# Kernel optimization log

Hardware: AMD Instinct MI355X
Metric: run time of the kernel (lower is better)

## Reference

```python
import jax, jax.numpy as jnp
import numpy as np

B, L, DIN, H, N, TEMB, NB = 16, 1024, 64, 256, 64, 128, 6


def setup_inputs() -> dict:
    key = jax.random.key(0)
    ks = jax.random.split(key, 16)
    def nrm(k, shape, scale):
        return jax.random.normal(k, shape, dtype=jnp.float32) * scale
    inp = {}
    inp["input"] = nrm(ks[0], (B, L, DIN), 1.0)
    inp["t"] = jax.random.uniform(ks[1], (B,), dtype=jnp.float32) * 1000.0
    inp["W_in"] = nrm(ks[2], (DIN, H), DIN ** -0.5)
    inp["b_in"] = jnp.zeros((H,), jnp.float32)
    inp["Wt1"] = nrm(ks[3], (TEMB, H), TEMB ** -0.5)
    inp["bt1"] = jnp.zeros((H,), jnp.float32)
    inp["Wt2"] = nrm(ks[4], (H, H), H ** -0.5)
    inp["bt2"] = jnp.zeros((H,), jnp.float32)
    inp["ln_g"] = jnp.ones((NB, H), jnp.float32)
    inp["ln_b"] = jnp.zeros((NB, H), jnp.float32)
    lo, hi = float(np.log(0.001)), float(np.log(0.1))
    inp["log_dt"] = jax.random.uniform(ks[5], (NB, H), dtype=jnp.float32) * (hi - lo) + lo
    inp["A_log_re"] = jnp.full((NB, H, N), float(np.log(0.5)), jnp.float32)
    inp["A_im"] = jnp.broadcast_to(np.pi * jnp.arange(N, dtype=jnp.float32), (NB, H, N)) + 0.0
    inp["C_re"] = nrm(ks[6], (NB, 2, H, N), 0.5 ** 0.5)
    inp["C_im"] = nrm(ks[7], (NB, 2, H, N), 0.5 ** 0.5)
    inp["Dp"] = nrm(ks[8], (NB, H), 1.0)
    inp["s4W"] = nrm(ks[9], (NB, H, H), H ** -0.5)
    inp["s4b"] = jnp.zeros((NB, H), jnp.float32)
    inp["tW"] = nrm(ks[10], (NB, H, H), H ** -0.5)
    inp["tb"] = jnp.zeros((NB, H), jnp.float32)
    inp["c1W"] = nrm(ks[11], (NB, H, H), H ** -0.5)
    inp["c1b"] = jnp.zeros((NB, H), jnp.float32)
    inp["c2W"] = nrm(ks[12], (NB, H, H), H ** -0.5)
    inp["c2b"] = jnp.zeros((NB, H), jnp.float32)
    inp["Wo1"] = nrm(ks[13], (H, H), H ** -0.5)
    inp["bo1"] = jnp.zeros((H,), jnp.float32)
    inp["Wo2"] = nrm(ks[14], (H, DIN), H ** -0.5)
    inp["bo2"] = jnp.zeros((DIN,), jnp.float32)
    return inp


def _sin_emb(t, dim):
    half = dim // 2
    freqs = jnp.exp(-np.log(10000.0) / (half - 1) * jnp.arange(half, dtype=jnp.float32))
    a = t[:, None] * freqs[None, :]
    return jnp.concatenate([jnp.sin(a), jnp.cos(a)], axis=-1)


def _forward(input, t, W_in, b_in, Wt1, bt1, Wt2, bt2, ln_g, ln_b, log_dt, A_log_re,
             A_im, C_re, C_im, Dp, s4W, s4b, tW, tb, c1W, c1b, c2W, c2b, Wo1, bo1, Wo2, bo2):
    x = jax.nn.relu(input @ W_in + b_in)                     # [B,L,H]
    tv = jax.nn.silu(_sin_emb(t, TEMB) @ Wt1 + bt1)
    tv = jax.nn.silu(tv @ Wt2 + bt2)                         # [B,H]
    x = jnp.swapaxes(x, -1, -2)                              # [B,H,L]
    length = x.shape[-1]
    nfft = 2 * length
    lgrid = jnp.arange(length)
    skips = jnp.zeros_like(x)
    for i in range(NB):
        # time conditioning (broadcast over L)
        tt = tv @ tW[i] + tb[i]                              # [B,H]
        z = x + tt[:, :, None]
        # LayerNorm over channel dim H
        zt = jnp.swapaxes(z, -1, -2)                         # [B,L,H]
        mu = zt.mean(-1, keepdims=True)
        var = zt.var(-1, keepdims=True)
        zn = (zt - mu) / jnp.sqrt(var + 1e-5) * ln_g[i] + ln_b[i]
        zn = jnp.swapaxes(zn, -1, -2)                        # [B,H,L]
        # S4 (diagonal ZOH) bidirectional convolution kernel
        dt = jnp.exp(log_dt[i])                              # [H]
        A = -jnp.exp(A_log_re[i]) + 1j * A_im[i]             # [H,N]
        dtA = A * dt[:, None]
        C = C_re[i] + 1j * C_im[i]                           # [2,H,N]
        dC = C * (jnp.exp(dtA) - 1.0) / A
        V = jnp.exp(dtA[:, :, None] * lgrid)                 # [H,N,L] Vandermonde
        K = 2.0 * jnp.einsum('shn,hnl->shl', dC, V).real     # [2,H,L]
        k = jnp.pad(K[0], ((0, 0), (0, length))) + jnp.pad(K[1][:, ::-1], ((0, 0), (length, 0)))
        y = jnp.fft.irfft(jnp.fft.rfft(zn, nfft) * jnp.fft.rfft(k, nfft)[None], nfft)[..., :length]
        y = y + zn * Dp[i][None, :, None]
        y = jax.nn.gelu(y, approximate=False)
        y = jnp.einsum('oh,bhl->bol', s4W[i], y) + s4b[i][None, :, None]
        out = y + z                                          # S4Layer residual
        g = jnp.tanh(out) * jax.nn.sigmoid(out)
        x = jnp.einsum('oh,bhl->bol', c1W[i], g) + c1b[i][None, :, None] + x
        skips = skips + jnp.einsum('oh,bhl->bol', c2W[i], g) + c2b[i][None, :, None]
    skip = jnp.swapaxes(skips, -1, -2)                       # [B,L,H]
    h = jax.nn.relu(skip @ Wo1 + bo1)
    out = h @ Wo2 + bo2
    return out + input                                       # init_skip


def reference(input, t, W_in, b_in, Wt1, bt1, Wt2, bt2, ln_g, ln_b, log_dt, A_log_re,
              A_im, C_re, C_im, Dp, s4W, s4b, tW, tb, c1W, c1b, c2W, c2b, Wo1, bo1, Wo2, bo2):
    return _forward(input, t, W_in, b_in, Wt1, bt1, Wt2, bt2, ln_g, ln_b, log_dt, A_log_re,
                    A_im, C_re, C_im, Dp, s4W, s4b, tW, tb, c1W, c1b, c2W, c2b, Wo1, bo1, Wo2, bo2)
```

## Files before the change

### kernel.cpp

```cpp
#include <hip/hip_runtime.h>
#include <math.h>


typedef __attribute__((ext_vector_type(8))) short bf16x8;
typedef __attribute__((ext_vector_type(4))) float f32x4;

__device__ __forceinline__ short f2bf(float f) {
  unsigned u = __builtin_bit_cast(unsigned, f);
  unsigned r = (u + 0x7FFFu + ((u >> 16) & 1u)) >> 16;
  return (short)r;
}
__device__ __forceinline__ float bf2f(unsigned short v) {
  unsigned u = ((unsigned)v) << 16;
  return __builtin_bit_cast(float, u);
}

__global__ __launch_bounds__(256) void k_temb(
    const float* __restrict__ t, const float* __restrict__ Wt1, const float* __restrict__ bt1,
    const float* __restrict__ Wt2, const float* __restrict__ bt2, float* __restrict__ tv) {
  int b = blockIdx.x, tid = threadIdx.x;
  __shared__ float emb[128];
  __shared__ float tv1[256];
  if (tid < 128) {
    int j = tid & 63;
// ... 14 lines not shown
__global__ __launch_bounds__(256) void k_tt(
    const float* __restrict__ tv, const float* __restrict__ tW, const float* __restrict__ tb,
    float* __restrict__ tt_all) {
  int i = blockIdx.x, b = blockIdx.y, h = threadIdx.x;
  __shared__ float s[256];
  s[h] = tv[b * 256 + h];
  __syncthreads();
  const float* W = tW + i * 256 * 256;
  float acc = tb[i * 256 + h];
  for (int k = 0; k < 256; k++) acc = fmaf(s[k], W[k * 256 + h], acc);
  tt_all[(i * 16 + b) * 256 + h] = acc;
}

__global__ __launch_bounds__(256) void k_in(
    const float* __restrict__ inp, const float* __restrict__ W, const float* __restrict__ bias,
    float* __restrict__ x) {
  int lt = blockIdx.x, b = blockIdx.y, h = threadIdx.x;
  __shared__ float si[64][68];
  int l0 = lt * 64;
  for (int rep = 0; rep < 16; rep++) {
    int idx = rep * 256 + h;
    int l = idx >> 6, d = idx & 63;
    si[l][d] = inp[(size_t)(b * 1024 + l0 + l) * 64 + d];
  }
  float wc[64];
  #pragma unroll
  for (int d = 0; d < 64; d++) wc[d] = W[d * 256 + h];
  float bh = bias[h];
  __syncthreads();
  float* xp = x + (size_t)(b * 256 + h) * 1024 + l0;
  for (int l4 = 0; l4 < 16; l4++) {
    float4 o;
    float* op = &o.x;
    #pragma unroll
    for (int j = 0; j < 4; j++) {
      int l = l4 * 4 + j;
      float a = bh;
      #pragma unroll
      for (int d4 = 0; d4 < 16; d4++) {
        float4 v = *reinterpret_cast<const float4*>(&si[l][d4 * 4]);
        a = fmaf(v.x, wc[d4 * 4 + 0], a);
        a = fmaf(v.y, wc[d4 * 4 + 1], a);
        a = fmaf(v.z, wc[d4 * 4 + 2], a);
        a = fmaf(v.w, wc[d4 * 4 + 3], a);
      }
      op[j] = fmaxf(a, 0.f);
    }
    *reinterpret_cast<float4*>(xp + l4 * 4) = o;
  }
}

__global__ __launch_bounds__(256) void k_tab(
    const float* __restrict__ log_dt, const float* __restrict__ A_log_re, const float* __restrict__ A_im,
    const float* __restrict__ C_re, const float* __restrict__ C_im,
    float* __restrict__ wtab, float* __restrict__ wTtab, float* __restrict__ dCtab) {
  int idx = blockIdx.x * 256 + threadIdx.x;
  int i = idx / (256 * 64);
  int rem = idx % (256 * 64);
  int h = rem >> 6, n = rem & 63;
  float dt = expf(log_dt[i * 256 + h]);
  float Ar = -expf(A_log_re[idx]);
  float Ai = A_im[idx];
  float ar = dt * Ar, ai = dt * Ai;
// ... 25 lines not shown
    s4Wbf[idx] = (unsigned short)f2bf(s4W[idx]);
  } else if (idx < 393216 + 786432) {
    int j = idx - 393216;
    int i = j / 131072, r = j % 131072;
    int o2 = r >> 8, k = r & 255;
    float v = (o2 < 256) ? c1W[(size_t)i * 65536 + o2 * 256 + k]
                         : c2W[(size_t)i * 65536 + (o2 - 256) * 256 + k];
    c12Wbf[j] = (unsigned short)f2bf(v);
  } else {
    int j = idx - 1179648;
    int o = j >> 8, k = j & 255;
    Wo1T[j] = (unsigned short)f2bf(Wo1[k * 256 + o]);
  }
}

__global__ __launch_bounds__(256) void k_conv(const float* __restrict__ src, unsigned short* __restrict__ dst) {
  int idx = (blockIdx.x * 256 + threadIdx.x) * 8;
  float4 v0 = *reinterpret_cast<const float4*>(src + idx);
  float4 v1 = *reinterpret_cast<const float4*>(src + idx + 4);
  ushort4 a = make_ushort4((unsigned short)f2bf(v0.x), (unsigned short)f2bf(v0.y),
                           (unsigned short)f2bf(v0.z), (unsigned short)f2bf(v0.w));
  ushort4 b = make_ushort4((unsigned short)f2bf(v1.x), (unsigned short)f2bf(v1.y),
                           (unsigned short)f2bf(v1.z), (unsigned short)f2bf(v1.w));
  *reinterpret_cast<ushort4*>(dst + idx) = a;
  *reinterpret_cast<ushort4*>(dst + idx + 4) = b;
}

__global__ __launch_bounds__(256) void k_pcar(const float* __restrict__ wtab, float* __restrict__ Pt) {
  int idx = blockIdx.x * 256 + threadIdx.x;
  int i = idx >> 14, h = (idx >> 6) & 255, n = idx & 63;
  float wr = wtab[idx * 2], wi = wtab[idx * 2 + 1];
  float pr = 1.f, pi = 0.f;
  float* base = Pt + (size_t)i * 2097152 + (size_t)h * 8192 + 2 * n;
  for (int t = 0; t < 64; t++) {
    *reinterpret_cast<float2*>(base + t * 128) = make_float2(pr, -pi);
    float nr2 = pr * wr - pi * wi, ni2 = pr * wi + pi * wr;
    pr = nr2; pi = ni2;
  }
}

__global__ __launch_bounds__(256) void k_ktap(
    const float* __restrict__ dCtab, const float* __restrict__ Pt, float* __restrict__ Ktap) {
  int idx = blockIdx.x * 256 + threadIdx.x;
  int j = idx & 63;
  int h = (idx >> 6) & 255;
  int i = idx >> 15;
  const float* dc = dCtab + (size_t)(idx >> 6) * 128;
  const float* P = Pt + (size_t)i * 2097152 + (size_t)h * 8192 + j * 128;
  float acc = 0.f;
  for (int q = 0; q < 32; q++) {
    float4 d = *reinterpret_cast<const float4*>(dc + q * 4);
    float4 p = *reinterpret_cast<const float4*>(P + q * 4);
    acc = fmaf(d.x, p.x, fmaf(d.y, p.y, fmaf(d.z, p.z, fmaf(d.w, p.w, acc))));
  }
  Ktap[idx] = 2.f * acc;
}

__global__ __launch_bounds__(256) void k_ln(
    const float* __restrict__ x, const float* __restrict__ tt_all,
    const float* __restrict__ g, const float* __restrict__ bta, unsigned short* __restrict__ znbf, int i) {
  int ct = blockIdx.x, b = blockIdx.y, tid = threadIdx.x;
  __shared__ float tile[64][257];
  __shared__ float stt[256];
  __shared__ float red[8][64];
  __shared__ float mu_s[64], rs_s[64];
  stt[tid] = tt_all[(i * 16 + b) * 256 + tid];
  __syncthreads();
  int l0 = ct * 64;
  const float* xb = x + (size_t)(b * 256) * 1024 + l0;
  for (int rep = 0; rep < 16; rep++) {
    int idx = rep * 256 + tid;
    int h = idx >> 4;
    int l4 = (idx & 15) * 4;
    float4 v = *reinterpret_cast<const float4*>(xb + (size_t)h * 1024 + l4);
    float a = stt[h];
    tile[l4][h] = v.x + a; tile[l4 + 1][h] = v.y + a; tile[l4 + 2][h] = v.z + a; tile[l4 + 3][h] = v.w + a;
  }
  __syncthreads();
  int l = tid & 63, part = tid >> 6;
  float s1 = 0.f, s2 = 0.f;
  for (int k = 0; k < 64; k++) {
    float v = tile[l][part * 64 + k];
    s1 += v; s2 = fmaf(v, v, s2);
  }
  red[part][l] = s1; red[4 + part][l] = s2;
  __syncthreads();
  if (tid < 64) {
    float a = red[0][tid] + red[1][tid] + red[2][tid] + red[3][tid];
    float q = red[4][tid] + red[5][tid] + red[6][tid] + red[7][tid];
    float mu = a * (1.f / 256.f);
    float var = q * (1.f / 256.f) - mu * mu;
    mu_s[tid] = mu;
    rs_s[tid] = rsqrtf(var + 1e-5f);
  }
  __syncthreads();
  unsigned short* zb = znbf + (size_t)(b * 256) * 1024 + l0;
  for (int rep = 0; rep < 16; rep++) {
    int idx = rep * 256 + tid;
    int h = idx >> 4;
    int l4 = (idx & 15) * 4;
    float gg = g[i * 256 + h], bb2 = bta[i * 256 + h];
    float o0 = (tile[l4][h]     - mu_s[l4])     * rs_s[l4]     * gg + bb2;
    float o1 = (tile[l4 + 1][h] - mu_s[l4 + 1]) * rs_s[l4 + 1] * gg + bb2;
    float o2 = (tile[l4 + 2][h] - mu_s[l4 + 2]) * rs_s[l4 + 2] * gg + bb2;
    float o3 = (tile[l4 + 3][h] - mu_s[l4 + 3]) * rs_s[l4 + 3] * gg + bb2;
    ushort4 o4 = make_ushort4((unsigned short)f2bf(o0), (unsigned short)f2bf(o1),
                              (unsigned short)f2bf(o2), (unsigned short)f2bf(o3));
    *reinterpret_cast<ushort4*>(zb + (size_t)h * 1024 + l4) = o4;
  }
}

__global__ __launch_bounds__(512, 1) void k_s4(
    const unsigned short* __restrict__ znbf, const float* __restrict__ Pt,
    const float* __restrict__ wtab, const float* __restrict__ wTtab, const float* __restrict__ dCtab,
    const float* __restrict__ Ktap, const float* __restrict__ Dp,
    unsigned short* __restrict__ ygbf, int i) {
  int h = blockIdx.x;
  int tid = threadIdx.x;
  __shared__ unsigned short Psb[64][130];
  __shared__ unsigned short XR[22016];
  __shared__ unsigned short Sw[8][2][16][136];
  __shared__ float k0s[64], k1s[64];

  if (tid < 64) k0s[tid] = Ktap[h * 64 + tid];
  else if (tid < 128) k1s[tid - 64] = Ktap[16384 + h * 64 + (tid - 64)];

  {
    const float* src = Pt + (size_t)h * 8192;
    #pragma unroll
    for (int rep = 0; rep < 4; rep++) {
      int idx = rep * 512 + tid;
      int t = idx >> 5, k4 = (idx & 31) * 4;
      float4 v = *reinterpret_cast<const float4*>(src + t * 128 + k4);
      ushort2 a = make_ushort2((unsigned short)f2bf(v.x), (unsigned short)f2bf(v.y));
      ushort2 bq = make_ushort2((unsigned short)f2bf(v.z), (unsigned short)f2bf(v.w));
      *reinterpret_cast<ushort2*>(&Psb[t][k4]) = a;
      *reinterpret_cast<ushort2*>(&Psb[t][k4 + 2]) = bq;
    }
  }
  __syncthreads();
  {
    int t = tid & 63;
    int colblk = tid >> 6;
    #pragma unroll
    for (int cc = 0; cc < 32; cc++) {
      int col = colblk * 32 + cc;
      int n = col & 63, comp = (col >> 6) & 1, dir = col >> 7;
      int k = 2 * n + comp;
      unsigned short v = dir ? Psb[t][k] : Psb[63 - t][k];
      if (comp) v ^= 0x8000u;
      XR[col * 72 + t] = v;
    }
  }
  __syncthreads();

  int wid = tid >> 6, lane = tid & 63;
  int b = blockIdx.y * 8 + wid;
  int c = lane & 15, kq = lane >> 4;
  const unsigned short* pzn = znbf + ((size_t)(b * 256 + h)) * 1024 + c * 64 + kq * 8;

  bf16x8 af0 = *reinterpret_cast<const bf16x8*>(pzn);
  bf16x8 af1 = *reinterpret_cast<const bf16x8*>(pzn + 32);

  f32x4 acc[16];
  #pragma unroll
  for (int nt = 0; nt < 16; nt++) acc[nt] = (f32x4){0.f, 0.f, 0.f, 0.f};
  #pragma unroll
  for (int nt = 0; nt < 16; nt++) {
    bf16x8 b0 = *reinterpret_cast<const bf16x8*>(&XR[(nt * 16 + c) * 72 + kq * 8]);
    acc[nt] = __builtin_amdgcn_mfma_f32_16x16x32_bf16(af0, b0, acc[nt], 0, 0, 0);
  }
  #pragma unroll
  for (int nt = 0; nt < 16; nt++) {
    bf16x8 b1 = *reinterpret_cast<const bf16x8*>(&XR[(nt * 16 + c) * 72 + 32 + kq * 8]);
    acc[nt] = __builtin_amdgcn_mfma_f32_16x16x32_bf16(af1, b1, acc[nt], 0, 0, 0);
  }
  __syncthreads();

  {
    int trow = tid >> 6, klane = tid & 63;
    #pragma unroll
    for (int ti = 0; ti < 8; ti++) {
      int t = ti * 8 + trow;
      #pragma unroll
      for (int kc = 0; kc < 5; kc++) {
        int k = kc * 64 + klane;
        unsigned short v;
        if (kc < 2)      v = Psb[t][k];
        else if (kc < 4) v = Psb[63 - t][k - 128];
        else {
          int tp = klane;
          float f = (t >= tp) ? k0s[t - tp] : k1s[tp - t - 1];
          v = (unsigned short)f2bf(f);
        }
        XR[t * 344 + k] = v;
      }
    }
  }

  unsigned short* swf = &Sw[wid][0][0][0];
  unsigned short* swb = &Sw[wid][1][0][0];
  const int gib = (i * 256 + h) * 64;
  #pragma unroll
  for (int j = 0; j < 4; j++) {
    int n = j * 16 + c;
    int gi = gib + n;
    float wTr = wTtab[gi * 2], wTi = wTtab[gi * 2 + 1];
    float w2r = wTr * wTr - wTi * wTi, w2i = 2.f * wTr * wTi;
    float w4r = w2r * w2r - w2i * w2i, w4i = 2.f * w2r * w2i;
    float w8r = w4r * w4r - w4i * w4i, w8i = 2.f * w4r * w4i;
    float wr = wtab[gi * 2], wi = wtab[gi * 2 + 1];
    float d0r = dCtab[((size_t)(i * 2 + 0) * 256 + h) * 128 + 2 * n];
    float d0i = dCtab[((size_t)(i * 2 + 0) * 256 + h) * 128 + 2 * n + 1];
    float d1r = dCtab[((size_t)(i * 2 + 1) * 256 + h) * 128 + 2 * n];
    float d1i = dCtab[((size_t)(i * 2 + 1) * 256 + h) * 128 + 2 * n + 1];
    float mfr = 2.f * (d0r * wr - d0i * wi), mfi = 2.f * (d0r * wi + d0i * wr);
    float mbr = 2.f * d1r, mbi = 2.f * d1i;

    {
      float er = 0.f, ei = 0.f, entr[4], enti[4];
      #pragma unroll
      for (int r = 0; r < 4; r++) {
        entr[r] = er; enti[r] = ei;
        float br = acc[j][r], bi = acc[j + 4][r];
        float t0 = er * wTr - ei * wTi + br;
        ei = er * wTi + ei * wTr + bi; er = t0;
      }
      float Gr = er, Gi = ei;
      float sr = __shfl_up(Gr, 16), si = __shfl_up(Gi, 16);
      if (kq >= 1) { Gr += sr * w4r - si * w4i; Gi += sr * w4i + si * w4r; }
      sr = __shfl_up(Gr, 32); si = __shfl_up(Gi, 32);
      if (kq >= 2) { Gr += sr * w8r - si * w8i; Gi += sr * w8i + si * w8r; }
      float Sgr = __shfl_up(Gr, 16), Sgi = __shfl_up(Gi, 16);
      if (kq == 0) { Sgr = 0.f; Sgi = 0.f; }
      float pr = 1.f, pi = 0.f;
      #pragma unroll
      for (int r = 0; r < 4; r++) {
        float scr = pr * Sgr - pi * Sgi + entr[r];
        float sci = pr * Sgi + pi * Sgr + enti[r];
        float opr = mfr * scr - mfi * sci;
        float opi = mfr * sci + mfi * scr;
        *reinterpret_cast<ushort2*>(swf + (kq * 4 + r) * 136 + 2 * n) =
            make_ushort2((unsigned short)f2bf(opr), (unsigned short)f2bf(opi));
        float t0 = pr * wTr - pi * wTi; pi = pr * wTi + pi * wTr; pr = t0;
      }
    }
    {
      float er = 0.f, ei = 0.f, entr[4], enti[4];
      #pragma unroll
      for (int rr = 0; rr < 4; rr++) {
        int r = 3 - rr;
        entr[r] = er; enti[r] = ei;
        float br = acc[8 + j][r], bi = acc[12 + j][r];
        float t0 = er * wTr - ei * wTi + br;
        ei = er * wTi + ei * wTr + bi; er = t0;
      }
      float Gr = er, Gi = ei;
      float sr = __shfl_down(Gr, 16), si = __shfl_down(Gi, 16);
      if (kq <= 2) { Gr += sr * w4r - si * w4i; Gi += sr * w4i + si * w4r; }
      sr = __shfl_down(Gr, 32); si = __shfl_down(Gi, 32);
      if (kq <= 1) { Gr += sr * w8r - si * w8i; Gi += sr * w8i + si * w8r; }
      float Sgr = __shfl_down(Gr, 16), Sgi = __shfl_down(Gi, 16);
      if (kq == 3) { Sgr = 0.f; Sgi = 0.f; }
      float pr = 1.f, pi = 0.f;
      #pragma unroll
      for (int rr = 0; rr < 4; rr++) {
        int r = 3 - rr;
        float scr = pr * Sgr - pi * Sgi + entr[r];
        float sci = pr * Sgi + pi * Sgr + enti[r];
        float opr = mbr * scr - mbi * sci;
        float opi = mbr * sci + mbi * scr;
        *reinterpret_cast<ushort2*>(swb + (kq * 4 + r) * 136 + 2 * n) =
            make_ushort2((unsigned short)f2bf(opr), (unsigned short)f2bf(opi));
        float t0 = pr * wTr - pi * wTi; pi = pr * wTi + pi * wTr; pr = t0;
      }
    }
  }
  __syncthreads();

  f32x4 acc2[4];
  #pragma unroll
  for (int nt = 0; nt < 4; nt++) acc2[nt] = (f32x4){0.f, 0.f, 0.f, 0.f};
  #pragma unroll
  for (int ks = 0; ks < 10; ks++) {
    bf16x8 af;
    if (ks < 4)       af = *reinterpret_cast<const bf16x8*>(swf + c * 136 + ks * 32 + kq * 8);
    else if (ks < 8)  af = *reinterpret_cast<const bf16x8*>(swb + c * 136 + (ks - 4) * 32 + kq * 8);
    else              af = *reinterpret_cast<const bf16x8*>(pzn + (ks - 8) * 32);
    #pragma unroll
    for (int nt = 0; nt < 4; nt++) {
      bf16x8 bfv = *reinterpret_cast<const bf16x8*>(&XR[(nt * 16 + c) * 344 + ks * 32 + kq * 8]);
      acc2[nt] = __builtin_amdgcn_mfma_f32_16x16x32_bf16(af, bfv, acc2[nt], 0, 0, 0);
    }
  }

  float dp = Dp[i * 256 + h];
  size_t obase = (size_t)(b * 256 + h) * 1024;
  #pragma unroll
  for (int nt = 0; nt < 4; nt++) {
    #pragma unroll
    for (int r = 0; r < 4; r++) {
      int m = kq * 4 + r;
      int t = nt * 16 + c;
      size_t idx = obase + (size_t)m * 64 + t;
      float z = bf2f(znbf[idx]);
      float v = fmaf(z, dp, acc2[nt][r]);
      float gel = 0.5f * v * (1.f + erff(v * 0.70710678118f));
      ygbf[idx] = (unsigned short)f2bf(gel);
    }
  }
}

template <int EPI>
__global__ __launch_bounds__(256) void k_gemm(
    const unsigned short* __restrict__ Wbf, const float* __restrict__ bias1, const float* __restrict__ bias2,
    const unsigned short* __restrict__ act, float* __restrict__ out1, float* __restrict__ out2,
    unsigned short* __restrict__ outb, const float* __restrict__ aux1, const float* __restrict__ aux2) {
  int lt = blockIdx.x, ot = blockIdx.y, b = blockIdx.z;
  int tid = threadIdx.x;
  int l0 = lt * 128, o0 = ot * 64;
  __shared__ unsigned short Alds[128 * 40];

  int wid = tid >> 6, lane = tid & 63;
  int wo = wid >> 1, wl = wid & 1;
  int c = lane & 15, kq = lane >> 4;

  int kq4 = tid >> 5;
  int lq = tid & 31;
  const unsigned short* actb = act + (size_t)(b * 256) * 1024 + l0 + lq * 4;

  f32x4 acc[2][4];
  #pragma unroll
// ... 50 lines not shown
        acc[mo][nl] = __builtin_amdgcn_mfma_f32_16x16x32_bf16(af[mo], bfr[nl], acc[mo][nl], 0, 0, 0);
    __syncthreads();
  }

  #pragma unroll
  for (int mo = 0; mo < 2; mo++) {
    #pragma unroll
    for (int nl = 0; nl < 4; nl++) {
      #pragma unroll
      for (int r = 0; r < 4; r++) {
        float a = acc[mo][nl][r];
        int o = o0 + wo * 32 + mo * 16 + kq * 4 + r;
        int l = l0 + wl * 64 + nl * 16 + c;
        if constexpr (EPI == 0) {
          size_t id = ((size_t)(b * 256 + o)) * 1024 + l;
          float u = a + bias1[o] + aux1[id] + aux2[b * 256 + o];
          float t = __expf(fminf(-u, 80.f));
          float gg = (1.f - t) / (1.f + t * t);
          outb[id] = (unsigned short)f2bf(gg);
        } else if constexpr (EPI == 1 || EPI == 4) {
          if (o < 256) {
            size_t id = ((size_t)(b * 256 + o)) * 1024 + l;
            out1[id] += a + bias1[o];
          } else {
            int o2 = o - 256;
            size_t id = ((size_t)(b * 256 + o2)) * 1024 + l;
            if constexpr (EPI == 4) out2[id] = a + bias2[o2];
            else                    out2[id] += a + bias2[o2];
          }
        } else {
          size_t id = ((size_t)(b * 256 + o)) * 1024 + l;
          out1[id] = fmaxf(a + bias1[o], 0.f);
        }
      }
    }
  }
}

__global__ __launch_bounds__(256) void k_out(
    const float* __restrict__ h1, const float* __restrict__ Wo2, const float* __restrict__ bo2,
    const float* __restrict__ inp, float* __restrict__ outp) {
  int lt = blockIdx.x, b = blockIdx.y, tid = threadIdx.x;
  __shared__ float sa[32][132];
  __shared__ float sw2[32][68];
  int l0 = lt * 128;
  float acc[4][8];
  #pragma unroll
  for (int r = 0; r < 4; r++)
    #pragma unroll
    for (int c2 = 0; c2 < 8; c2++) acc[r][c2] = 0.f;
  int df = (tid & 7) * 8;
  int lf = (tid >> 3) * 4;
  for (int kc = 0; kc < 256; kc += 32) {
    for (int rep = 0; rep < 4; rep++) {
      int idx = rep * 256 + tid;
      int kk = idx >> 5;
      int l4 = (idx & 31) * 4;
      float4 v = *reinterpret_cast<const float4*>(h1 + (size_t)(b * 256 + kc + kk) * 1024 + l0 + l4);
      *reinterpret_cast<float4*>(&sa[kk][l4]) = v;
    }
    for (int rep = 0; rep < 8; rep++) {
      int idx = rep * 256 + tid;
      int kk = idx >> 6, d = idx & 63;
      sw2[kk][d] = Wo2[(size_t)(kc + kk) * 64 + d];
    }
    __syncthreads();
    for (int kk = 0; kk < 32; kk++) {
      float4 av = *reinterpret_cast<const float4*>(&sa[kk][lf]);
      float4 w1 = *reinterpret_cast<const float4*>(&sw2[kk][df]);
      float4 w2 = *reinterpret_cast<const float4*>(&sw2[kk][df + 4]);
      float avv[4] = {av.x, av.y, av.z, av.w};
      float wv[8] = {w1.x, w1.y, w1.z, w1.w, w2.x, w2.y, w2.z, w2.w};
      #pragma unroll
      for (int r = 0; r < 4; r++)
// ... 41 lines not shown
  const float* s4W     = (const float*)d_in[16];
  const float* s4b     = (const float*)d_in[17];
  const float* tW      = (const float*)d_in[18];
  const float* tb      = (const float*)d_in[19];
  const float* c1W     = (const float*)d_in[20];
  const float* c1b     = (const float*)d_in[21];
  const float* c2W     = (const float*)d_in[22];
  const float* c2b     = (const float*)d_in[23];
  const float* Wo1     = (const float*)d_in[24];
  const float* bo1     = (const float*)d_in[25];
  const float* Wo2     = (const float*)d_in[26];
  const float* bo2     = (const float*)d_in[27];

  float* ws = (float*)d_ws;
  size_t off = 0;
  float* x      = ws + off; off += 4194304;
  float* zn     = ws + off; off += 4194304;
  float* ygbuf  = ws + off; off += 4194304;
  float* skips  = ws + off; off += 4194304;
  float* tv     = ws + off; off += 4096;
  float* tt_all = ws + off; off += 24576;
  float* wtab   = ws + off; off += 196608;
  float* wTtab  = ws + off; off += 196608;
  float* dCtab  = ws + off; off += 393216;
  float* Pt     = ws + off; off += 12582912;
  float* Ktap   = ws + off; off += 196608;
  unsigned short* s4Wbf  = (unsigned short*)(ws + off); off += 196608;
  unsigned short* c12Wbf = (unsigned short*)(ws + off); off += 393216;
  unsigned short* Wo1T   = (unsigned short*)(ws + off); off += 32768;

  unsigned short* znbf    = (unsigned short*)zn;
  unsigned short* ygbf    = (unsigned short*)ygbuf;
  unsigned short* gbf     = (unsigned short*)(ygbuf + 2097152);
  unsigned short* skipsbf = (unsigned short*)x;
  float* h1 = zn;

  k_temb<<<16, 256, 0, stream>>>(t, Wt1, bt1, Wt2, bt2, tv);
  k_tt<<<dim3(6, 16), 256, 0, stream>>>(tv, tW, tb, tt_all);
  k_in<<<dim3(16, 16), 256, 0, stream>>>(input, W_in, b_in, x);
  k_tab<<<384, 256, 0, stream>>>(log_dt, A_log_re, A_im, C_re, C_im, wtab, wTtab, dCtab);
  k_prep<<<4864, 256, 0, stream>>>(s4W, c1W, c2W, Wo1, s4Wbf, c12Wbf, Wo1T);
  k_pcar<<<384, 256, 0, stream>>>(wtab, Pt);
  k_ktap<<<768, 256, 0, stream>>>(dCtab, Pt, Ktap);

  for (int i = 0; i < 6; i++) {
    k_ln<<<dim3(16, 16), 256, 0, stream>>>(x, tt_all, ln_g, ln_b, znbf, i);
    k_s4<<<dim3(256, 2), 512, 0, stream>>>(znbf, Pt + (size_t)i * 2097152, wtab, wTtab, dCtab,
                                           Ktap + (size_t)i * 32768, Dp, ygbf, i);
    k_gemm<0><<<dim3(8, 4, 16), 256, 0, stream>>>(s4Wbf + (size_t)i * 65536, s4b + i * 256, nullptr,
                                                  ygbf, nullptr, nullptr, gbf, x, tt_all + i * 4096);
    if (i == 0)
      k_gemm<4><<<dim3(8, 8, 16), 256, 0, stream>>>(c12Wbf, c1b, c2b, gbf, x, skips,
                                                    nullptr, nullptr, nullptr);
    else
      k_gemm<1><<<dim3(8, 8, 16), 256, 0, stream>>>(c12Wbf + (size_t)i * 131072, c1b + i * 256,
                                                    c2b + i * 256, gbf, x, skips,
                                                    nullptr, nullptr, nullptr);
  }
  k_conv<<<2048, 256, 0, stream>>>(skips, skipsbf);
  k_gemm<2><<<dim3(8, 4, 16), 256, 0, stream>>>(Wo1T, bo1, nullptr,
                                                skipsbf, h1, nullptr, nullptr, nullptr, nullptr);
  k_out<<<dim3(8, 16), 256, 0, stream>>>(h1, Wo2, bo2, input, (float*)d_out);
}
```

Measured before the change: 580.2 us.

## Store residual, skip, and S4 power tables in bf16 and restructure S4 blocks

The residual stream x, the skip accumulator, h1, and the Pt power table are now stored as bf16 instead of fp32. This roughly halves global memory traffic in the LN, GEMM epilogue, S4, and output kernels and removes the separate skip-conversion kernel. The S4 kernel now launches one block per channel that handles both batch halves, so the Pt/Toeplitz shared-memory setup is built once and reused. The cost is accuracy: the residual and skip sums are re-rounded to bf16 after every layer's accumulation, which may drift beyond tolerance.

Measured after the change: 790.0 us. 1.36x slower.

```diff
diff --git a/kernel.cpp b/kernel.cpp
--- a/kernel.cpp
+++ b/kernel.cpp
@@ -52,7 +52,7 @@
 
 __global__ __launch_bounds__(256) void k_in(
     const float* __restrict__ inp, const float* __restrict__ W, const float* __restrict__ bias,
-    float* __restrict__ x) {
+    unsigned short* __restrict__ xbf) {
   int lt = blockIdx.x, b = blockIdx.y, h = threadIdx.x;
   __shared__ float si[64][68];
   int l0 = lt * 64;
@@ -66,10 +66,9 @@
   for (int d = 0; d < 64; d++) wc[d] = W[d * 256 + h];
   float bh = bias[h];
   __syncthreads();
-  float* xp = x + (size_t)(b * 256 + h) * 1024 + l0;
+  unsigned short* xp = xbf + (size_t)(b * 256 + h) * 1024 + l0;
   for (int l4 = 0; l4 < 16; l4++) {
-    float4 o;
-    float* op = &o.x;
+    float op[4];
     #pragma unroll
     for (int j = 0; j < 4; j++) {
       int l = l4 * 4 + j;
@@ -84,7 +83,9 @@
       }
       op[j] = fmaxf(a, 0.f);
     }
-    *reinterpret_cast<float4*>(xp + l4 * 4) = o;
+    ushort4 o = make_ushort4((unsigned short)f2bf(op[0]), (unsigned short)f2bf(op[1]),
+                             (unsigned short)f2bf(op[2]), (unsigned short)f2bf(op[3]));
+    *reinterpret_cast<ushort4*>(xp + l4 * 4) = o;
   }
 }
 
@@ -140,73 +141,65 @@
   }
 }
 
-__global__ __launch_bounds__(256) void k_conv(const float* __restrict__ src, unsigned short* __restrict__ dst) {
-  int idx = (blockIdx.x * 256 + threadIdx.x) * 8;
-  float4 v0 = *reinterpret_cast<const float4*>(src + idx);
-  float4 v1 = *reinterpret_cast<const float4*>(src + idx + 4);
-  ushort4 a = make_ushort4((unsigned short)f2bf(v0.x), (unsigned short)f2bf(v0.y),
-                           (unsigned short)f2bf(v0.z), (unsigned short)f2bf(v0.w));
-  ushort4 b = make_ushort4((unsigned short)f2bf(v1.x), (unsigned short)f2bf(v1.y),
-                           (unsigned short)f2bf(v1.z), (unsigned short)f2bf(v1.w));
-  *reinterpret_cast<ushort4*>(dst + idx) = a;
-  *reinterpret_cast<ushort4*>(dst + idx + 4) = b;
-}
-
-__global__ __launch_bounds__(256) void k_pcar(const float* __restrict__ wtab, float* __restrict__ Pt) {
+__global__ __launch_bounds__(256) void k_pcar(const float* __restrict__ wtab, unsigned short* __restrict__ Ptb) {
   int idx = blockIdx.x * 256 + threadIdx.x;
   int i = idx >> 14, h = (idx >> 6) & 255, n = idx & 63;
   float wr = wtab[idx * 2], wi = wtab[idx * 2 + 1];
   float pr = 1.f, pi = 0.f;
-  float* base = Pt + (size_t)i * 2097152 + (size_t)h * 8192 + 2 * n;
+  unsigned short* base = Ptb + (size_t)i * 2097152 + (size_t)h * 8192 + 2 * n;
   for (int t = 0; t < 64; t++) {
-    *reinterpret_cast<float2*>(base + t * 128) = make_float2(pr, -pi);
+    *reinterpret_cast<ushort2*>(base + t * 128) =
+        make_ushort2((unsigned short)f2bf(pr), (unsigned short)f2bf(-pi));
     float nr2 = pr * wr - pi * wi, ni2 = pr * wi + pi * wr;
     pr = nr2; pi = ni2;
   }
 }
 
 __global__ __launch_bounds__(256) void k_ktap(
-    const float* __restrict__ dCtab, const float* __restrict__ Pt, float* __restrict__ Ktap) {
+    const float* __restrict__ dCtab, const unsigned short* __restrict__ Ptb, float* __restrict__ Ktap) {
   int idx = blockIdx.x * 256 + threadIdx.x;
   int j = idx & 63;
   int h = (idx >> 6) & 255;
   int i = idx >> 15;
   const float* dc = dCtab + (size_t)(idx >> 6) * 128;
-  const float* P = Pt + (size_t)i * 2097152 + (size_t)h * 8192 + j * 128;
+  const unsigned short* P = Ptb + (size_t)i * 2097152 + (size_t)h * 8192 + j * 128;
   float acc = 0.f;
   for (int q = 0; q < 32; q++) {
     float4 d = *reinterpret_cast<const float4*>(dc + q * 4);
-    float4 p = *reinterpret_cast<const float4*>(P + q * 4);
-    acc = fmaf(d.x, p.x, fmaf(d.y, p.y, fmaf(d.z, p.z, fmaf(d.w, p.w, acc))));
+    ushort4 p = *reinterpret_cast<const ushort4*>(P + q * 4);
+    acc = fmaf(d.x, bf2f(p.x), fmaf(d.y, bf2f(p.y), fmaf(d.z, bf2f(p.z), fmaf(d.w, bf2f(p.w), acc))));
   }
   Ktap[idx] = 2.f * acc;
 }
 
 __global__ __launch_bounds__(256) void k_ln(
-    const float* __restrict__ x, const float* __restrict__ tt_all,
+    const unsigned short* __restrict__ xbf, const float* __restrict__ tt_all,
     const float* __restrict__ g, const float* __restrict__ bta, unsigned short* __restrict__ znbf, int i) {
   int ct = blockIdx.x, b = blockIdx.y, tid = threadIdx.x;
-  __shared__ float tile[64][257];
+  __shared__ unsigned short tile[64][266];
   __shared__ float stt[256];
   __shared__ float red[8][64];
   __shared__ float mu_s[64], rs_s[64];
   stt[tid] = tt_all[(i * 16 + b) * 256 + tid];
   __syncthreads();
   int l0 = ct * 64;
-  const float* xb = x + (size_t)(b * 256) * 1024 + l0;
+  const unsigned short* xb = xbf + (size_t)(b * 256) * 1024 + l0;
   for (int rep = 0; rep < 16; rep++) {
     int idx = rep * 256 + tid;
     int h = idx >> 4;
     int l4 = (idx & 15) * 4;
-    float4 v = *reinterpret_cast<const float4*>(xb + (size_t)h * 1024 + l4);
+    ushort4 v = *reinterpret_cast<const ushort4*>(xb + (size_t)h * 1024 + l4);
     float a = stt[h];
-    tile[l4][h] = v.x + a; tile[l4 + 1][h] = v.y + a; tile[l4 + 2][h] = v.z + a; tile[l4 + 3][h] = v.w + a;
+    tile[l4][h]     = (unsigned short)f2bf(bf2f(v.x) + a);
+    tile[l4 + 1][h] = (unsigned short)f2bf(bf2f(v.y) + a);
+    tile[l4 + 2][h] = (unsigned short)f2bf(bf2f(v.z) + a);
+    tile[l4 + 3][h] = (unsigned short)f2bf(bf2f(v.w) + a);
   }
   __syncthreads();
   int l = tid & 63, part = tid >> 6;
   float s1 = 0.f, s2 = 0.f;
   for (int k = 0; k < 64; k++) {
-    float v = tile[l][part * 64 + k];
+    float v = bf2f(tile[l][part * 64 + k]);
     s1 += v; s2 = fmaf(v, v, s2);
   }
   red[part][l] = s1; red[4 + part][l] = s2;
@@ -226,10 +219,10 @@
     int h = idx >> 4;
     int l4 = (idx & 15) * 4;
     float gg = g[i * 256 + h], bb2 = bta[i * 256 + h];
-    float o0 = (tile[l4][h]     - mu_s[l4])     * rs_s[l4]     * gg + bb2;
-    float o1 = (tile[l4 + 1][h] - mu_s[l4 + 1]) * rs_s[l4 + 1] * gg + bb2;
-    float o2 = (tile[l4 + 2][h] - mu_s[l4 + 2]) * rs_s[l4 + 2] * gg + bb2;
-    float o3 = (tile[l4 + 3][h] - mu_s[l4 + 3]) * rs_s[l4 + 3] * gg + bb2;
+    float o0 = (bf2f(tile[l4][h])     - mu_s[l4])     * rs_s[l4]     * gg + bb2;
+    float o1 = (bf2f(tile[l4 + 1][h]) - mu_s[l4 + 1]) * rs_s[l4 + 1] * gg + bb2;
+    float o2 = (bf2f(tile[l4 + 2][h]) - mu_s[l4 + 2]) * rs_s[l4 + 2] * gg + bb2;
+    float o3 = (bf2f(tile[l4 + 3][h]) - mu_s[l4 + 3]) * rs_s[l4 + 3] * gg + bb2;
     ushort4 o4 = make_ushort4((unsigned short)f2bf(o0), (unsigned short)f2bf(o1),
                               (unsigned short)f2bf(o2), (unsigned short)f2bf(o3));
     *reinterpret_cast<ushort4*>(zb + (size_t)h * 1024 + l4) = o4;
@@ -237,31 +230,28 @@
 }
 
 __global__ __launch_bounds__(512, 1) void k_s4(
-    const unsigned short* __restrict__ znbf, const float* __restrict__ Pt,
+    const unsigned short* __restrict__ znbf, const unsigned short* __restrict__ Ptb,
     const float* __restrict__ wtab, const float* __restrict__ wTtab, const float* __restrict__ dCtab,
     const float* __restrict__ Ktap, const float* __restrict__ Dp,
     unsigned short* __restrict__ ygbf, int i) {
   int h = blockIdx.x;
   int tid = threadIdx.x;
-  __shared__ unsigned short Psb[64][130];
-  __shared__ unsigned short XR[22016];
-  __shared__ unsigned short Sw[8][2][16][136];
+  __shared__ unsigned short Bp[256 * 72];
+  __shared__ unsigned short Blds[64 * 344];
+  __shared__ unsigned short SwA[34816];
   __shared__ float k0s[64], k1s[64];
 
   if (tid < 64) k0s[tid] = Ktap[h * 64 + tid];
   else if (tid < 128) k1s[tid - 64] = Ktap[16384 + h * 64 + (tid - 64)];
 
   {
-    const float* src = Pt + (size_t)h * 8192;
+    const unsigned short* src = Ptb + (size_t)h * 8192;
     #pragma unroll
     for (int rep = 0; rep < 4; rep++) {
-      int idx = rep * 512 + tid;
-      int t = idx >> 5, k4 = (idx & 31) * 4;
-      float4 v = *reinterpret_cast<const float4*>(src + t * 128 + k4);
-      ushort2 a = make_ushort2((unsigned short)f2bf(v.x), (unsigned short)f2bf(v.y));
-      ushort2 bq = make_ushort2((unsigned short)f2bf(v.z), (unsigned short)f2bf(v.w));
-      *reinterpret_cast<ushort2*>(&Psb[t][k4]) = a;
-      *reinterpret_cast<ushort2*>(&Psb[t][k4 + 2]) = bq;
+      int idx4 = (rep * 512 + tid) * 4;
+      int t = idx4 >> 7, k = idx4 & 127;
+      ushort4 v = *reinterpret_cast<const ushort4*>(src + idx4);
+      *reinterpret_cast<ushort4*>(&SwA[t * 132 + k]) = v;
     }
   }
   __syncthreads();
@@ -273,60 +263,38 @@
       int col = colblk * 32 + cc;
       int n = col & 63, comp = (col >> 6) & 1, dir = col >> 7;
       int k = 2 * n + comp;
-      unsigned short v = dir ? Psb[t][k] : Psb[63 - t][k];
+      unsigned short v = dir ? SwA[t * 132 + k] : SwA[(63 - t) * 132 + k];
       if (comp) v ^= 0x8000u;
-      XR[col * 72 + t] = v;
-    }
-  }
-  __syncthreads();
-
-  int wid = tid >> 6, lane = tid & 63;
-  int b = blockIdx.y * 8 + wid;
-  int c = lane & 15, kq = lane >> 4;
-  const unsigned short* pzn = znbf + ((size_t)(b * 256 + h)) * 1024 + c * 64 + kq * 8;
-
-  bf16x8 af0 = *reinterpret_cast<const bf16x8*>(pzn);
-  bf16x8 af1 = *reinterpret_cast<const bf16x8*>(pzn + 32);
-
-  f32x4 acc[16];
-  #pragma unroll
-  for (int nt = 0; nt < 16; nt++) acc[nt] = (f32x4){0.f, 0.f, 0.f, 0.f};
-  #pragma unroll
-  for (int nt = 0; nt < 16; nt++) {
-    bf16x8 b0 = *reinterpret_cast<const bf16x8*>(&XR[(nt * 16 + c) * 72 + kq * 8]);
-    acc[nt] = __builtin_amdgcn_mfma_f32_16x16x32_bf16(af0, b0, acc[nt], 0, 0, 0);
-  }
-  #pragma unroll
-  for (int nt = 0; nt < 16; nt++) {
-    bf16x8 b1 = *reinterpret_cast<const bf16x8*>(&XR[(nt * 16 + c) * 72 + 32 + kq * 8]);
-    acc[nt] = __builtin_amdgcn_mfma_f32_16x16x32_bf16(af1, b1, acc[nt], 0, 0, 0);
-  }
-  __syncthreads();
-
-  {
+      Bp[col * 72 + t] = v;
+    }
     int trow = tid >> 6, klane = tid & 63;
     #pragma unroll
     for (int ti = 0; ti < 8; ti++) {
-      int t = ti * 8 + trow;
+      int t2 = ti * 8 + trow;
       #pragma unroll
       for (int kc = 0; kc < 5; kc++) {
         int k = kc * 64 + klane;
         unsigned short v;
-        if (kc < 2)      v = Psb[t][k];
-        else if (kc < 4) v = Psb[63 - t][k - 128];
+        if (kc < 2)      v = SwA[t2 * 132 + k];
+        else if (kc < 4) v = SwA[(63 - t2) * 132 + (k - 128)];
         else {
           int tp = klane;
-          float f = (t >= tp) ? k0s[t - tp] : k1s[tp - t - 1];
+          float f = (t2 >= tp) ? k0s[t2 - tp] : k1s[tp - t2 - 1];
           v = (unsigned short)f2bf(f);
         }
-        XR[t * 344 + k] = v;
+        Blds[t2 * 344 + k] = v;
       }
     }
   }
-
-  unsigned short* swf = &Sw[wid][0][0][0];
-  unsigned short* swb = &Sw[wid][1][0][0];
+  __syncthreads();
+
+  int wid = tid >> 6, lane = tid & 63;
+  int c = lane & 15, kq = lane >> 4;
+  unsigned short* swf = &SwA[(wid * 2 + 0) * 2176];
+  unsigned short* swb = &SwA[(wid * 2 + 1) * 2176];
   const int gib = (i * 256 + h) * 64;
+
+  float wTr_[4], wTi_[4], w4r_[4], w4i_[4], w8r_[4], w8i_[4], mfr_[4], mfi_[4], mbr_[4], mbi_[4];
   #pragma unroll
   for (int j = 0; j < 4; j++) {
     int n = j * 16 + c;
@@ -334,105 +302,134 @@
     float wTr = wTtab[gi * 2], wTi = wTtab[gi * 2 + 1];
     float w2r = wTr * wTr - wTi * wTi, w2i = 2.f * wTr * wTi;
     float w4r = w2r * w2r - w2i * w2i, w4i = 2.f * w2r * w2i;
-    float w8r = w4r * w4r - w4i * w4i, w8i = 2.f * w4r * w4i;
+    w8r_[j] = w4r * w4r - w4i * w4i; w8i_[j] = 2.f * w4r * w4i;
+    w4r_[j] = w4r; w4i_[j] = w4i;
+    wTr_[j] = wTr; wTi_[j] = wTi;
     float wr = wtab[gi * 2], wi = wtab[gi * 2 + 1];
     float d0r = dCtab[((size_t)(i * 2 + 0) * 256 + h) * 128 + 2 * n];
     float d0i = dCtab[((size_t)(i * 2 + 0) * 256 + h) * 128 + 2 * n + 1];
     float d1r = dCtab[((size_t)(i * 2 + 1) * 256 + h) * 128 + 2 * n];
     float d1i = dCtab[((size_t)(i * 2 + 1) * 256 + h) * 128 + 2 * n + 1];
-    float mfr = 2.f * (d0r * wr - d0i * wi), mfi = 2.f * (d0r * wi + d0i * wr);
-    float mbr = 2.f * d1r, mbi = 2.f * d1i;
-
-    {
-      float er = 0.f, ei = 0.f, entr[4], enti[4];
+    mfr_[j] = 2.f * (d0r * wr - d0i * wi); mfi_[j] = 2.f * (d0r * wi + d0i * wr);
+    mbr_[j] = 2.f * d1r; mbi_[j] = 2.f * d1i;
+  }
+  float dp = Dp[i * 256 + h];
+
+  for (int bq = 0; bq < 2; bq++) {
+    int b = bq * 8 + wid;
+    const unsigned short* pzn = znbf + ((size_t)(b * 256 + h)) * 1024 + c * 64 + kq * 8;
+    bf16x8 af0 = *reinterpret_cast<const bf16x8*>(pzn);
+    bf16x8 af1 = *reinterpret_cast<const bf16x8*>(pzn + 32);
+
+    f32x4 acc[16];
+    #pragma unroll
+    for (int nt = 0; nt < 16; nt++) acc[nt] = (f32x4){0.f, 0.f, 0.f, 0.f};
+    #pragma unroll
+    for (int nt = 0; nt < 16; nt++) {
+      bf16x8 b0 = *reinterpret_cast<const bf16x8*>(&Bp[(nt * 16 + c) * 72 + kq * 8]);
+      acc[nt] = __builtin_amdgcn_mfma_f32_16x16x32_bf16(af0, b0, acc[nt], 0, 0, 0);
+    }
+    #pragma unroll
+    for (int nt = 0; nt < 16; nt++) {
+      bf16x8 b1 = *reinterpret_cast<const bf16x8*>(&Bp[(nt * 16 + c) * 72 + 32 + kq * 8]);
+      acc[nt] = __builtin_amdgcn_mfma_f32_16x16x32_bf16(af1, b1, acc[nt], 0, 0, 0);
+    }
+
+    #pragma unroll
+    for (int j = 0; j < 4; j++) {
+      int n = j * 16 + c;
+      float wTr = wTr_[j], wTi = wTi_[j];
+      float w4r = w4r_[j], w4i = w4i_[j], w8r = w8r_[j], w8i = w8i_[j];
+      float mfr = mfr_[j], mfi = mfi_[j], mbr = mbr_[j], mbi = mbi_[j];
+      {
+        float er = 0.f, ei = 0.f, entr[4], enti[4];
+        #pragma unroll
+        for (int r = 0; r < 4; r++) {
+          entr[r] = er; enti[r] = ei;
+          float br = acc[j][r], bi = acc[j + 4][r];
+          float t0 = er * wTr - ei * wTi + br;
+          ei = er * wTi + ei * wTr + bi; er = t0;
+        }
+        float Gr = er, Gi = ei;
+        float sr = __shfl_up(Gr, 16), si = __shfl_up(Gi, 16);
+        if (kq >= 1) { Gr += sr * w4r - si * w4i; Gi += sr * w4i + si * w4r; }
+        sr = __shfl_up(Gr, 32); si = __shfl_up(Gi, 32);
+        if (kq >= 2) { Gr += sr * w8r - si * w8i; Gi += sr * w8i + si * w8r; }
+        float Sgr = __shfl_up(Gr, 16), Sgi = __shfl_up(Gi, 16);
+        if (kq == 0) { Sgr = 0.f; Sgi = 0.f; }
+        float pr = 1.f, pi = 0.f;
+        #pragma unroll
+        for (int r = 0; r < 4; r++) {
+          float scr = pr * Sgr - pi * Sgi + entr[r];
+          float sci = pr * Sgi + pi * Sgr + enti[r];
+          float opr = mfr * scr - mfi * sci;
+          float opi = mfr * sci + mfi * scr;
+          *reinterpret_cast<ushort2*>(swf + (kq * 4 + r) * 136 + 2 * n) =
+              make_ushort2((unsigned short)f2bf(opr), (unsigned short)f2bf(opi));
+          float t0 = pr * wTr - pi * wTi; pi = pr * wTi + pi * wTr; pr = t0;
+        }
+      }
+      {
+        float er = 0.f, ei = 0.f, entr[4], enti[4];
+        #pragma unroll
+        for (int rr = 0; rr < 4; rr++) {
+          int r = 3 - rr;
+          entr[r] = er; enti[r] = ei;
+          float br = acc[8 + j][r], bi = acc[12 + j][r];
+          float t0 = er * wTr - ei * wTi + br;
+          ei = er * wTi + ei * wTr + bi; er = t0;
+        }
+        float Gr = er, Gi = ei;
+        float sr = __shfl_down(Gr, 16), si = __shfl_down(Gi, 16);
+        if (kq <= 2) { Gr += sr * w4r - si * w4i; Gi += sr * w4i + si * w4r; }
+        sr = __shfl_down(Gr, 32); si = __shfl_down(Gi, 32);
+        if (kq <= 1) { Gr += sr * w8r - si * w8i; Gi += sr * w8i + si * w8r; }
+        float Sgr = __shfl_down(Gr, 16), Sgi = __shfl_down(Gi, 16);
+        if (kq == 3) { Sgr = 0.f; Sgi = 0.f; }
+        float pr = 1.f, pi = 0.f;
+        #pragma unroll
+        for (int rr = 0; rr < 4; rr++) {
+          int r = 3 - rr;
+          float scr = pr * Sgr - pi * Sgi + entr[r];
+          float sci = pr * Sgi + pi * Sgr + enti[r];
+          float opr = mbr * scr - mbi * sci;
+          float opi = mbr * sci + mbi * scr;
+          *reinterpret_cast<ushort2*>(swb + (kq * 4 + r) * 136 + 2 * n) =
+              make_ushort2((unsigned short)f2bf(opr), (unsigned short)f2bf(opi));
+          float t0 = pr * wTr - pi * wTi; pi = pr * wTi + pi * wTr; pr = t0;
+        }
+      }
+    }
+
+    f32x4 acc2[4];
+    #pragma unroll
+    for (int nt = 0; nt < 4; nt++) acc2[nt] = (f32x4){0.f, 0.f, 0.f, 0.f};
+    #pragma unroll
+    for (int ks = 0; ks < 10; ks++) {
+      bf16x8 af;
+      if (ks < 4)       af = *reinterpret_cast<const bf16x8*>(swf + c * 136 + ks * 32 + kq * 8);
+      else if (ks < 8)  af = *reinterpret_cast<const bf16x8*>(swb + c * 136 + (ks - 4) * 32 + kq * 8);
+      else              af = *reinterpret_cast<const bf16x8*>(pzn + (ks - 8) * 32);
+      #pragma unroll
+      for (int nt = 0; nt < 4; nt++) {
+        bf16x8 bfv = *reinterpret_cast<const bf16x8*>(&Blds[(nt * 16 + c) * 344 + ks * 32 + kq * 8]);
+        acc2[nt] = __builtin_amdgcn_mfma_f32_16x16x32_bf16(af, bfv, acc2[nt], 0, 0, 0);
+      }
+    }
+
+    size_t obase = (size_t)(b * 256 + h) * 1024;
+    #pragma unroll
+    for (int nt = 0; nt < 4; nt++) {
       #pragma unroll
       for (int r = 0; r < 4; r++) {
-        entr[r] = er; enti[r] = ei;
-        float br = acc[j][r], bi = acc[j + 4][r];
-        float t0 = er * wTr - ei * wTi + br;
-        ei = er * wTi + ei * wTr + bi; er = t0;
+        int m = kq * 4 + r;
+        int t = nt * 16 + c;
+        size_t idx = obase + (size_t)m * 64 + t;
+        float z = bf2f(znbf[idx]);
+        float v = fmaf(z, dp, acc2[nt][r]);
+        float gel = 0.5f * v * (1.f + erff(v * 0.70710678118f));
+        ygbf[idx] = (unsigned short)f2bf(gel);
       }
-      float Gr = er, Gi = ei;
-      float sr = __shfl_up(Gr, 16), si = __shfl_up(Gi, 16);
-      if (kq >= 1) { Gr += sr * w4r - si * w4i; Gi += sr * w4i + si * w4r; }
-      sr = __shfl_up(Gr, 32); si = __shfl_up(Gi, 32);
-      if (kq >= 2) { Gr += sr * w8r - si * w8i; Gi += sr * w8i + si * w8r; }
-      float Sgr = __shfl_up(Gr, 16), Sgi = __shfl_up(Gi, 16);
-      if (kq == 0) { Sgr = 0.f; Sgi = 0.f; }
-      float pr = 1.f, pi = 0.f;
-      #pragma unroll
-      for (int r = 0; r < 4; r++) {
-        float scr = pr * Sgr - pi * Sgi + entr[r];
-        float sci = pr * Sgi + pi * Sgr + enti[r];
-        float opr = mfr * scr - mfi * sci;
-        float opi = mfr * sci + mfi * scr;
-        *reinterpret_cast<ushort2*>(swf + (kq * 4 + r) * 136 + 2 * n) =
-            make_ushort2((unsigned short)f2bf(opr), (unsigned short)f2bf(opi));
-        float t0 = pr * wTr - pi * wTi; pi = pr * wTi + pi * wTr; pr = t0;
-      }
-    }
-    {
-      float er = 0.f, ei = 0.f, entr[4], enti[4];
-      #pragma unroll
-      for (int rr = 0; rr < 4; rr++) {
-        int r = 3 - rr;
-        entr[r] = er; enti[r] = ei;
-        float br = acc[8 + j][r], bi = acc[12 + j][r];
-        float t0 = er * wTr - ei * wTi + br;
-        ei = er * wTi + ei * wTr + bi; er = t0;
-      }
-      float Gr = er, Gi = ei;
-      float sr = __shfl_down(Gr, 16), si = __shfl_down(Gi, 16);
-      if (kq <= 2) { Gr += sr * w4r - si * w4i; Gi += sr * w4i + si * w4r; }
-      sr = __shfl_down(Gr, 32); si = __shfl_down(Gi, 32);
-      if (kq <= 1) { Gr += sr * w8r - si * w8i; Gi += sr * w8i + si * w8r; }
-      float Sgr = __shfl_down(Gr, 16), Sgi = __shfl_down(Gi, 16);
-      if (kq == 3) { Sgr = 0.f; Sgi = 0.f; }
-      float pr = 1.f, pi = 0.f;
-      #pragma unroll
-      for (int rr = 0; rr < 4; rr++) {
-        int r = 3 - rr;
-        float scr = pr * Sgr - pi * Sgi + entr[r];
-        float sci = pr * Sgi + pi * Sgr + enti[r];
-        float opr = mbr * scr - mbi * sci;
-        float opi = mbr * sci + mbi * scr;
-        *reinterpret_cast<ushort2*>(swb + (kq * 4 + r) * 136 + 2 * n) =
-            make_ushort2((unsigned short)f2bf(opr), (unsigned short)f2bf(opi));
-        float t0 = pr * wTr - pi * wTi; pi = pr * wTi + pi * wTr; pr = t0;
-      }
-    }
-  }
-  __syncthreads();
-
-  f32x4 acc2[4];
-  #pragma unroll
-  for (int nt = 0; nt < 4; nt++) acc2[nt] = (f32x4){0.f, 0.f, 0.f, 0.f};
-  #pragma unroll
-  for (int ks = 0; ks < 10; ks++) {
-    bf16x8 af;
-    if (ks < 4)       af = *reinterpret_cast<const bf16x8*>(swf + c * 136 + ks * 32 + kq * 8);
-    else if (ks < 8)  af = *reinterpret_cast<const bf16x8*>(swb + c * 136 + (ks - 4) * 32 + kq * 8);
-    else              af = *reinterpret_cast<const bf16x8*>(pzn + (ks - 8) * 32);
-    #pragma unroll
-    for (int nt = 0; nt < 4; nt++) {
-      bf16x8 bfv = *reinterpret_cast<const bf16x8*>(&XR[(nt * 16 + c) * 344 + ks * 32 + kq * 8]);
-      acc2[nt] = __builtin_amdgcn_mfma_f32_16x16x32_bf16(af, bfv, acc2[nt], 0, 0, 0);
-    }
-  }
-
-  float dp = Dp[i * 256 + h];
-  size_t obase = (size_t)(b * 256 + h) * 1024;
-  #pragma unroll
-  for (int nt = 0; nt < 4; nt++) {
-    #pragma unroll
-    for (int r = 0; r < 4; r++) {
-      int m = kq * 4 + r;
-      int t = nt * 16 + c;
-      size_t idx = obase + (size_t)m * 64 + t;
-      float z = bf2f(znbf[idx]);
-      float v = fmaf(z, dp, acc2[nt][r]);
-      float gel = 0.5f * v * (1.f + erff(v * 0.70710678118f));
-      ygbf[idx] = (unsigned short)f2bf(gel);
     }
   }
 }
@@ -440,8 +437,8 @@
 template <int EPI>
 __global__ __launch_bounds__(256) void k_gemm(
     const unsigned short* __restrict__ Wbf, const float* __restrict__ bias1, const float* __restrict__ bias2,
-    const unsigned short* __restrict__ act, float* __restrict__ out1, float* __restrict__ out2,
-    unsigned short* __restrict__ outb, const float* __restrict__ aux1, const float* __restrict__ aux2) {
+    const unsigned short* __restrict__ act, unsigned short* __restrict__ uio1, unsigned short* __restrict__ uio2,
+    unsigned short* __restrict__ outb, const unsigned short* __restrict__ aux1, const float* __restrict__ aux2) {
   int lt = blockIdx.x, ot = blockIdx.y, b = blockIdx.z;
   int tid = threadIdx.x;
   int l0 = lt * 128, o0 = ot * 64;
@@ -522,23 +519,23 @@
         int l = l0 + wl * 64 + nl * 16 + c;
         if constexpr (EPI == 0) {
           size_t id = ((size_t)(b * 256 + o)) * 1024 + l;
-          float u = a + bias1[o] + aux1[id] + aux2[b * 256 + o];
+          float u = a + bias1[o] + bf2f(aux1[id]) + aux2[b * 256 + o];
           float t = __expf(fminf(-u, 80.f));
           float gg = (1.f - t) / (1.f + t * t);
           outb[id] = (unsigned short)f2bf(gg);
         } else if constexpr (EPI == 1 || EPI == 4) {
           if (o < 256) {
             size_t id = ((size_t)(b * 256 + o)) * 1024 + l;
-            out1[id] += a + bias1[o];
+            uio1[id] = (unsigned short)f2bf(bf2f(uio1[id]) + a + bias1[o]);
           } else {
             int o2 = o - 256;
             size_t id = ((size_t)(b * 256 + o2)) * 1024 + l;
-            if constexpr (EPI == 4) out2[id] = a + bias2[o2];
-            else                    out2[id] += a + bias2[o2];
+            if constexpr (EPI == 4) uio2[id] = (unsigned short)f2bf(a + bias2[o2]);
+            else                    uio2[id] = (unsigned short)f2bf(bf2f(uio2[id]) + a + bias2[o2]);
           }
         } else {
           size_t id = ((size_t)(b * 256 + o)) * 1024 + l;
-          out1[id] = fmaxf(a + bias1[o], 0.f);
+          outb[id] = (unsigned short)f2bf(fmaxf(a + bias1[o], 0.f));
         }
       }
     }
@@ -546,7 +543,7 @@
 }
 
 __global__ __launch_bounds__(256) void k_out(
-    const float* __restrict__ h1, const float* __restrict__ Wo2, const float* __restrict__ bo2,
+    const unsigned short* __restrict__ h1, const float* __restrict__ Wo2, const float* __restrict__ bo2,
     const float* __restrict__ inp, float* __restrict__ outp) {
   int lt = blockIdx.x, b = blockIdx.y, tid = threadIdx.x;
   __shared__ float sa[32][132];
@@ -564,8 +561,9 @@
       int idx = rep * 256 + tid;
       int kk = idx >> 5;
       int l4 = (idx & 31) * 4;
-      float4 v = *reinterpret_cast<const float4*>(h1 + (size_t)(b * 256 + kc + kk) * 1024 + l0 + l4);
-      *reinterpret_cast<float4*>(&sa[kk][l4]) = v;
+      ushort4 v = *reinterpret_cast<const ushort4*>(h1 + (size_t)(b * 256 + kc + kk) * 1024 + l0 + l4);
+      sa[kk][l4] = bf2f(v.x); sa[kk][l4 + 1] = bf2f(v.y);
+      sa[kk][l4 + 2] = bf2f(v.z); sa[kk][l4 + 3] = bf2f(v.w);
     }
     for (int rep = 0; rep < 8; rep++) {
       int idx = rep * 256 + tid;
@@ -637,51 +635,52 @@
 
   float* ws = (float*)d_ws;
   size_t off = 0;
-  float* x      = ws + off; off += 4194304;
-  float* zn     = ws + off; off += 4194304;
+  float* xbuf   = ws + off; off += 4194304;
+  float* znbuf  = ws + off; off += 4194304;
   float* ygbuf  = ws + off; off += 4194304;
-  float* skips  = ws + off; off += 4194304;
+  float* skbuf  = ws + off; off += 4194304;
   float* tv     = ws + off; off += 4096;
   float* tt_all = ws + off; off += 24576;
   float* wtab   = ws + off; off += 196608;
   float* wTtab  = ws + off; off += 196608;
   float* dCtab  = ws + off; off += 393216;
-  float* Pt     = ws + off; off += 12582912;
+  float* Ptbuf  = ws + off; off += 6291456;
   float* Ktap   = ws + off; off += 196608;
   unsigned short* s4Wbf  = (unsigned short*)(ws + off); off += 196608;
   unsigned short* c12Wbf = (unsigned short*)(ws + off); off += 393216;
   unsigned short* Wo1T   = (unsigned short*)(ws + off); off += 32768;
 
-  unsigned short* znbf    = (unsigned short*)zn;
+  unsigned short* xbf     = (unsigned short*)xbuf;
+  unsigned short* znbf    = (unsigned short*)znbuf;
   unsigned short* ygbf    = (unsigned short*)ygbuf;
   unsigned short* gbf     = (unsigned short*)(ygbuf + 2097152);
-  unsigned short* skipsbf = (unsigned short*)x;
-  float* h1 = zn;
+  unsigned short* skipsbf = (unsigned short*)skbuf;
+  unsigned short* Ptb     = (unsigned short*)Ptbuf;
+  unsigned short* h1bf    = (unsigned short*)znbuf;
 
   k_temb<<<16, 256, 0, stream>>>(t, Wt1, bt1, Wt2, bt2, tv);
   k_tt<<<dim3(6, 16), 256, 0, stream>>>(tv, tW, tb, tt_all);
-  k_in<<<dim3(16, 16), 256, 0, stream>>>(input, W_in, b_in, x);
+  k_in<<<dim3(16, 16), 256, 0, stream>>>(input, W_in, b_in, xbf);
   k_tab<<<384, 256, 0, stream>>>(log_dt, A_log_re, A_im, C_re, C_im, wtab, wTtab, dCtab);
   k_prep<<<4864, 256, 0, stream>>>(s4W, c1W, c2W, Wo1, s4Wbf, c12Wbf, Wo1T);
-  k_pcar<<<384, 256, 0, stream>>>(wtab, Pt);
-  k_ktap<<<768, 256, 0, stream>>>(dCtab, Pt, Ktap);
+  k_pcar<<<384, 256, 0, stream>>>(wtab, Ptb);
+  k_ktap<<<768, 256, 0, stream>>>(dCtab, Ptb, Ktap);
 
   for (int i = 0; i < 6; i++) {
-    k_ln<<<dim3(16, 16), 256, 0, stream>>>(x, tt_all, ln_g, ln_b, znbf, i);
-    k_s4<<<dim3(256, 2), 512, 0, stream>>>(znbf, Pt + (size_t)i * 2097152, wtab, wTtab, dCtab,
-                                           Ktap + (size_t)i * 32768, Dp, ygbf, i);
+    k_ln<<<dim3(16, 16), 256, 0, stream>>>(xbf, tt_all, ln_g, ln_b, znbf, i);
+    k_s4<<<256, 512, 0, stream>>>(znbf, Ptb + (size_t)i * 2097152, wtab, wTtab, dCtab,
+                                  Ktap + (size_t)i * 32768, Dp, ygbf, i);
     k_gemm<0><<<dim3(8, 4, 16), 256, 0, stream>>>(s4Wbf + (size_t)i * 65536, s4b + i * 256, nullptr,
-                                                  ygbf, nullptr, nullptr, gbf, x, tt_all + i * 4096);
+                                                  ygbf, nullptr, nullptr, gbf, xbf, tt_all + i * 4096);
     if (i == 0)
-      k_gemm<4><<<dim3(8, 8, 16), 256, 0, stream>>>(c12Wbf, c1b, c2b, gbf, x, skips,
+      k_gemm<4><<<dim3(8, 8, 16), 256, 0, stream>>>(c12Wbf, c1b, c2b, gbf, xbf, skipsbf,
                                                     nullptr, nullptr, nullptr);
     else
       k_gemm<1><<<dim3(8, 8, 16), 256, 0, stream>>>(c12Wbf + (size_t)i * 131072, c1b + i * 256,
-                                                    c2b + i * 256, gbf, x, skips,
+                                                    c2b + i * 256, gbf, xbf, skipsbf,
                                                     nullptr, nullptr, nullptr);
   }
-  k_conv<<<2048, 256, 0, stream>>>(skips, skipsbf);
   k_gemm<2><<<dim3(8, 4, 16), 256, 0, stream>>>(Wo1T, bo1, nullptr,
-                                                skipsbf, h1, nullptr, nullptr, nullptr, nullptr);
-  k_out<<<dim3(8, 16), 256, 0, stream>>>(h1, Wo2, bo2, input, (float*)d_out);
-}
+                                                skipsbf, nullptr, nullptr, h1bf, nullptr, nullptr);
+  k_out<<<dim3(8, 16), 256, 0, stream>>>(h1bf, Wo2, bo2, input, (float*)d_out);
+}
```
